# Performance work log

Measured on AMD Instinct MI355X. Metric: run time of the kernel, lower is better.

Reference implementation:

```python
import jax, jax.numpy as jnp
import numpy as np

# init kwargs baked as constants: crop_height -> depth dim, crop_length -> H, crop_width -> W
CROP_D, CROP_H, CROP_W = 16, 16, 16
EXTRAP = 0.0


def setup_inputs() -> dict:
    key = jax.random.key(0)
    k1, k2, k3 = jax.random.split(key, 3)
    N, C, D, H, W = 8, 32, 64, 64, 64
    NB = 256
    image = jax.random.normal(k1, (N, C, D, H, W), dtype=jnp.float32)
    # boxes: normalized (x1, y1, z1, x2, y2, z2) with lo <= hi per axis
    raw = jax.random.uniform(k2, (NB, 3, 2), dtype=jnp.float32)
    lo = jnp.min(raw, axis=2)
    hi = jnp.max(raw, axis=2)
    boxes = jnp.concatenate([lo, hi], axis=1)  # [NB, 6]
    box_ind = jax.random.randint(k3, (NB,), 0, N, dtype=jnp.int32)
    return {"image": image, "boxes": boxes, "box_ind": box_ind}


def _coords(lo, hi, L, c):
    # lo, hi: [nb] normalized box edges; returns [nb, c] continuous source coords
    if c > 1:
        i = jnp.arange(c, dtype=lo.dtype)
        step = (hi - lo) * (L - 1) / (c - 1)          # [nb]
        return lo[:, None] * (L - 1) + i[None, :] * step[:, None]
    return (0.5 * (lo + hi) * (L - 1))[:, None]


def _lerp_idx(coord, L):
    valid = (coord >= 0) & (coord <= L - 1)
    c = jnp.clip(coord, 0, L - 1)
    i0 = jnp.floor(c).astype(jnp.int32)
    i1 = jnp.minimum(i0 + 1, L - 1)
    frac = c - i0.astype(coord.dtype)
    return i0, i1, frac, valid


def reference(image, boxes, box_ind):
    N, C, D, H, W = image.shape
    x1, y1, z1, x2, y2, z2 = [boxes[:, k] for k in range(6)]
    zc = _coords(z1, z2, D, CROP_D)  # [nb, cd]
    yc = _coords(y1, y2, H, CROP_H)  # [nb, ch]
    xc = _coords(x1, x2, W, CROP_W)  # [nb, cw]
    z0, z1i, fz, vz = _lerp_idx(zc, D)
    y0, y1i, fy, vy = _lerp_idx(yc, H)
    x0, x1i, fx, vx = _lerp_idx(xc, W)

    img = jnp.moveaxis(image, 1, -1)  # [N, D, H, W, C] -> channels-last gather
    b = box_ind[:, None, None, None]

    def g(zi, yi, xi):
        # [nb, cd, ch, cw, C]
        return img[b, zi[:, :, None, None], yi[:, None, :, None], xi[:, None, None, :], :]

    fz_ = fz[:, :, None, None, None]
    fy_ = fy[:, None, :, None, None]
    fx_ = fx[:, None, None, :, None]

    c00 = g(z0, y0, x0) * (1 - fx_) + g(z0, y0, x1i) * fx_
    c01 = g(z0, y1i, x0) * (1 - fx_) + g(z0, y1i, x1i) * fx_
    c10 = g(z1i, y0, x0) * (1 - fx_) + g(z1i, y0, x1i) * fx_
    c11 = g(z1i, y1i, x0) * (1 - fx_) + g(z1i, y1i, x1i) * fx_
    c0 = c00 * (1 - fy_) + c01 * fy_
    c1 = c10 * (1 - fy_) + c11 * fy_
    out = c0 * (1 - fz_) + c1 * fz_  # [nb, cd, ch, cw, C]

    valid = (vz[:, :, None, None] & vy[:, None, :, None] & vx[:, None, None, :])[..., None]
    out = jnp.where(valid, out, jnp.asarray(EXTRAP, out.dtype))
    return jnp.moveaxis(out, -1, 1)  # [nb, C, cd, ch, cw]
```

## Files before the change

kernel.cpp:

```cpp
#include <hip/hip_runtime.h>
#include <stdint.h>

#define NBOX 256
#define NC   32
#define ND   64
#define NH   64
#define NW   64
#define CD   16
#define CH   16
#define CW   16
#define NXCD 8
#define DHW  (ND * NH * NW)

__global__ __launch_bounds__(NBOX) void CropAndResize3D_perm_kernel(
    const int* __restrict__ box_ind, int* __restrict__ perm)
{
    __shared__ int nsh[NBOX];
    const int t = threadIdx.x;
    nsh[t] = box_ind[t];
    __syncthreads();
    const int n_t = nsh[t];
    int rank = 0;
    #pragma unroll 8
    for (int j = 0; j < NBOX; ++j) {
        const int n_j = nsh[j];
        rank += (n_j < n_t) || (n_j == n_t && j < t);
    }
    perm[rank] = t;
}

__global__ __launch_bounds__(256) void CropAndResize3D_89481348645400_kernel(
    const float* __restrict__ image,
    const float* __restrict__ boxes,
    const int*   __restrict__ box_ind,
    const int*   __restrict__ perm,
    float*       __restrict__ out)
{
    __shared__ float sh[2 * 64 * 64];

    const int nwg_per_xcd = (NBOX * CD) / NXCD;
    const int hw  = blockIdx.x;
    const int blk = (hw & (NXCD - 1)) * nwg_per_xcd + (hw >> 3);

    const int slot = blk >> 4;
    const int b = perm ? perm[slot] : slot;
    const int z = blk & 15;
    const int t  = threadIdx.x;
    const int ty = t >> 4;
    const int tx = t & 15;

    const float bx1 = boxes[b*6+0], by1 = boxes[b*6+1], bz1 = boxes[b*6+2];
    const float bx2 = boxes[b*6+3], by2 = boxes[b*6+4], bz2 = boxes[b*6+5];
    const int   n   = box_ind[b];

    const float zstep = (bz2 - bz1) * 63.0f / 15.0f;
    const float ystep = (by2 - by1) * 63.0f / 15.0f;
    const float xstep = (bx2 - bx1) * 63.0f / 15.0f;

    const float zc = bz1 * 63.0f + (float)z * zstep;
    const bool  vz = (zc >= 0.0f) && (zc <= 63.0f);
    const float zq = fminf(fmaxf(zc, 0.0f), 63.0f);
    const int   z0 = (int)floorf(zq);
    const int   z1 = min(z0 + 1, ND - 1);
    const float fz = zq - (float)z0;

    const float yc = by1 * 63.0f + (float)ty * ystep;
    const bool  vy = (yc >= 0.0f) && (yc <= 63.0f);
    const float yq = fminf(fmaxf(yc, 0.0f), 63.0f);
    const float fy = yq - floorf(yq);

    const float xcf = bx1 * 63.0f + (float)tx * xstep;
    const bool  vx  = (xcf >= 0.0f) && (xcf <= 63.0f);
    const float xq  = fminf(fmaxf(xcf, 0.0f), 63.0f);
    const int   x0  = (int)floorf(xq);
    const int   x1  = min(x0 + 1, NW - 1);
    const float fx  = xq - (float)x0;

    const bool valid = vz && vy && vx;
    const float gz = 1.0f - fz, gy = 1.0f - fy, gx = 1.0f - fx;

    const float xcl = bx1 * 63.0f;
    const float xch = bx1 * 63.0f + 15.0f * xstep;
    const int x0min = (int)floorf(fminf(fmaxf(xcl, 0.0f), 63.0f));
    const int x1max = min((int)floorf(fminf(fmaxf(xch, 0.0f), 63.0f)) + 1, NW - 1);
    const int xlo4  = x0min & ~3;
    const int G     = ((x1max - xlo4) >> 2) + 1;

    const int key = ty & 7;
    const bool act = ((tx ^ key) < G);
    const int sx  = xlo4 + ((tx ^ key) << 2);

    int soff0, soff1, soff2, soff3;
    {
        int tmp[4];
        #pragma unroll
        for (int k = 0; k < 4; ++k) {
            const int r   = k * 16 + ty;
            const int yo  = (r >> 1) & 15;
            const int yc_ = r & 1;
            const int zs  = (r >> 5) ? z1 : z0;
            const float yco = by1 * 63.0f + (float)yo * ystep;
            const float yqs = fminf(fmaxf(yco, 0.0f), 63.0f);
            const int   ys0 = (int)floorf(yqs);
            const int   ysel = yc_ ? min(ys0 + 1, NH - 1) : ys0;
            tmp[k] = (zs * NH + ysel) * NW + sx;
        }
        soff0 = tmp[0]; soff1 = tmp[1]; soff2 = tmp[2]; soff3 = tmp[3];
    }
    const int wb    = (ty & ~3) * 64;
    const int ldsb0 = wb;
    const int ldsb1 = wb + 16 * 64;
    const int ldsb2 = wb + 32 * 64;
    const int ldsb3 = wb + 48 * 64;

    const int dx0 = x0 - xlo4;
    const int dx1 = x1 - xlo4;
    #define IDX(r, dx) ((r) * 64 + (((((dx) >> 2) ^ ((r) & 7))) << 2) + ((dx) & 3))
    const int a000 = IDX(2*ty    , dx0), a001 = IDX(2*ty    , dx1);
    const int a010 = IDX(2*ty + 1, dx0), a011 = IDX(2*ty + 1, dx1);
    const int a100 = IDX(32+2*ty , dx0), a101 = IDX(32+2*ty , dx1);
    const int a110 = IDX(33+2*ty , dx0), a111 = IDX(33+2*ty , dx1);
    #undef IDX

    const float* imgb = image + (size_t)n * (NC * DHW);
    float* op = out + (size_t)b * (NC * CD * CH * CW) + (z * CH + ty) * CW + tx;

    #define ISSUE(c)  do { if (act) {                                          \
        const float* p_ = imgb + (size_t)(c) * DHW;                            \
        float* l_ = sh + (((c) & 1) << 12);                                    \
        __builtin_amdgcn_global_load_lds(                                      \
            (const __attribute__((address_space(1))) uint32_t*)(p_ + soff0),   \
            (__attribute__((address_space(3))) uint32_t*)(l_ + ldsb0), 16, 0, 0); \
        __builtin_amdgcn_global_load_lds(                                      \
            (const __attribute__((address_space(1))) uint32_t*)(p_ + soff1),   \
            (__attribute__((address_space(3))) uint32_t*)(l_ + ldsb1), 16, 0, 0); \
        __builtin_amdgcn_global_load_lds(                                      \
            (const __attribute__((address_space(1))) uint32_t*)(p_ + soff2),   \
            (__attribute__((address_space(3))) uint32_t*)(l_ + ldsb2), 16, 0, 0); \
        __builtin_amdgcn_global_load_lds(                                      \
            (const __attribute__((address_space(1))) uint32_t*)(p_ + soff3),   \
            (__attribute__((address_space(3))) uint32_t*)(l_ + ldsb3), 16, 0, 0); \
    } } while (0)

    #define COMPUTE(c)  do {                                                   \
        const float* S_ = sh + (((c) & 1) << 12);                              \
        const float s000 = S_[a000], s001 = S_[a001];                          \
        const float s010 = S_[a010], s011 = S_[a011];                          \
        const float s100 = S_[a100], s101 = S_[a101];                          \
        const float s110 = S_[a110], s111 = S_[a111];                          \
        const float c00 = s000 * gx + s001 * fx;                               \
        const float c01 = s010 * gx + s011 * fx;                               \
        const float c10 = s100 * gx + s101 * fx;                               \
        const float c11 = s110 * gx + s111 * fx;                               \
        const float c0  = c00 * gy + c01 * fy;                                 \
        const float c1  = c10 * gy + c11 * fy;                                 \
        float v = c0 * gz + c1 * fz;                                           \
        v = valid ? v : 0.0f;                                                  \
        __builtin_nontemporal_store(v, op + (c) * (CD * CH * CW));             \
    } while (0)

    ISSUE(0);
    ISSUE(1);
    asm volatile("s_waitcnt vmcnt(4)" ::: "memory");
    __builtin_amdgcn_s_barrier();
    __builtin_amdgcn_sched_barrier(0);

    #pragma unroll 2
    for (int c = 0; c < NC; ++c) {
        COMPUTE(c);
        if (c + 1 < NC) {
            __builtin_amdgcn_sched_barrier(0);
            __builtin_amdgcn_s_barrier();
            __builtin_amdgcn_sched_barrier(0);
            if (c + 2 < NC) {
                ISSUE(c + 2);
                asm volatile("s_waitcnt vmcnt(4)" ::: "memory");
            } else {
                asm volatile("s_waitcnt vmcnt(0)" ::: "memory");
            }
            __builtin_amdgcn_sched_barrier(0);
            __builtin_amdgcn_s_barrier();
            __builtin_amdgcn_sched_barrier(0);
        }
    }

    #undef ISSUE
    #undef COMPUTE
}

extern "C" void kernel_launch(void* const* d_in, const int* in_sizes, int n_in,
                              void* d_out, int out_size, void* d_ws, size_t ws_size,
                              hipStream_t stream) {
    const float* image   = (const float*)d_in[0];
    const float* boxes   = (const float*)d_in[1];
    const int*   box_ind = (const int*)d_in[2];
    float*       out     = (float*)d_out;

    int* perm = nullptr;
    if (ws_size >= NBOX * sizeof(int)) {
        perm = (int*)d_ws;
        CropAndResize3D_perm_kernel<<<1, NBOX, 0, stream>>>(box_ind, perm);
    }

    const int blocks = NBOX * CD;
    CropAndResize3D_89481348645400_kernel<<<blocks, 256, 0, stream>>>(
        image, boxes, box_ind, perm, out);
}
```

Baseline: 112.1 us.

## Make LDS staging wave-private to drop workgroup barriers in channel loop

Remaps threads so each wave loads exactly the LDS rows it later reads (its 4 output rows across both z planes), making the double-buffered staging wave-local. This lets the per-channel s_barrier pairs be replaced with per-wave vmcnt/lgkmcnt waits, fully unrolls the loop, and has inactive lanes issue redundant clamped loads instead of being predicated off. The aim is to remove workgroup-wide synchronisation stalls, at the cost of some extra redundant global loads and a correctness dependence on exact vmcnt accounting, including the nontemporal stores.

```diff
diff --git a/kernel.cpp b/kernel.cpp
--- a/kernel.cpp
+++ b/kernel.cpp
@@ -39,15 +39,18 @@
     __shared__ float sh[2 * 64 * 64];
 
     const int nwg_per_xcd = (NBOX * CD) / NXCD;
-    const int hw  = blockIdx.x;
-    const int blk = (hw & (NXCD - 1)) * nwg_per_xcd + (hw >> 3);
+    const int hwid = blockIdx.x;
+    const int blk = (hwid & (NXCD - 1)) * nwg_per_xcd + (hwid >> 3);
 
     const int slot = blk >> 4;
     const int b = perm ? perm[slot] : slot;
     const int z = blk & 15;
     const int t  = threadIdx.x;
-    const int ty = t >> 4;
-    const int tx = t & 15;
+    const int w  = t >> 6;
+    const int l  = t & 63;
+    const int q  = l >> 4;
+    const int tx = l & 15;
+    const int ty = (w << 2) | q;
 
     const float bx1 = boxes[b*6+0], by1 = boxes[b*6+1], bz1 = boxes[b*6+2];
     const float bx2 = boxes[b*6+3], by2 = boxes[b*6+4], bz2 = boxes[b*6+5];
@@ -86,68 +89,65 @@
     const int xlo4  = x0min & ~3;
     const int G     = ((x1max - xlo4) >> 2) + 1;
 
-    const int key = ty & 7;
-    const bool act = ((tx ^ key) < G);
-    const int sx  = xlo4 + ((tx ^ key) << 2);
-
     int soff0, soff1, soff2, soff3;
     {
         int tmp[4];
         #pragma unroll
         for (int k = 0; k < 4; ++k) {
-            const int r   = k * 16 + ty;
-            const int yo  = (r >> 1) & 15;
-            const int yc_ = r & 1;
-            const int zs  = (r >> 5) ? z1 : z0;
+            const int rho = k * 4 + q;
+            const int zc_ = rho >> 3;
+            const int qq  = (rho >> 1) & 3;
+            const int yc_ = rho & 1;
+            const int zs  = zc_ ? z1 : z0;
+            const int yo  = (w << 2) | qq;
             const float yco = by1 * 63.0f + (float)yo * ystep;
             const float yqs = fminf(fmaxf(yco, 0.0f), 63.0f);
             const int   ys0 = (int)floorf(yqs);
             const int   ysel = yc_ ? min(ys0 + 1, NH - 1) : ys0;
+            const int   key = rho & 7;
+            const int   g   = tx ^ key;
+            const int   sx  = (g < G) ? (xlo4 + (g << 2)) : xlo4;
             tmp[k] = (zs * NH + ysel) * NW + sx;
         }
         soff0 = tmp[0]; soff1 = tmp[1]; soff2 = tmp[2]; soff3 = tmp[3];
     }
-    const int wb    = (ty & ~3) * 64;
-    const int ldsb0 = wb;
-    const int ldsb1 = wb + 16 * 64;
-    const int ldsb2 = wb + 32 * 64;
-    const int ldsb3 = wb + 48 * 64;
+    const int wbF = w << 10;
 
     const int dx0 = x0 - xlo4;
     const int dx1 = x1 - xlo4;
-    #define IDX(r, dx) ((r) * 64 + (((((dx) >> 2) ^ ((r) & 7))) << 2) + ((dx) & 3))
-    const int a000 = IDX(2*ty    , dx0), a001 = IDX(2*ty    , dx1);
-    const int a010 = IDX(2*ty + 1, dx0), a011 = IDX(2*ty + 1, dx1);
-    const int a100 = IDX(32+2*ty , dx0), a101 = IDX(32+2*ty , dx1);
-    const int a110 = IDX(33+2*ty , dx0), a111 = IDX(33+2*ty , dx1);
-    #undef IDX
+    #define SWZ(rho, dx) ((((((dx) >> 2) ^ ((rho) & 7))) << 2) | ((dx) & 3))
+    const int a000 = wbF + (2*q    ) * 64 + SWZ(2*q    , dx0);
+    const int a001 = wbF + (2*q    ) * 64 + SWZ(2*q    , dx1);
+    const int a010 = wbF + (2*q + 1) * 64 + SWZ(2*q + 1, dx0);
+    const int a011 = wbF + (2*q + 1) * 64 + SWZ(2*q + 1, dx1);
+    #undef SWZ
 
     const float* imgb = image + (size_t)n * (NC * DHW);
     float* op = out + (size_t)b * (NC * CD * CH * CW) + (z * CH + ty) * CW + tx;
 
-    #define ISSUE(c)  do { if (act) {                                          \
+    #define ISSUE(c)  do {                                                     \
         const float* p_ = imgb + (size_t)(c) * DHW;                            \
-        float* l_ = sh + (((c) & 1) << 12);                                    \
+        float* l_ = sh + (((c) & 1) << 12) + wbF;                              \
         __builtin_amdgcn_global_load_lds(                                      \
             (const __attribute__((address_space(1))) uint32_t*)(p_ + soff0),   \
-            (__attribute__((address_space(3))) uint32_t*)(l_ + ldsb0), 16, 0, 0); \
+            (__attribute__((address_space(3))) uint32_t*)(l_      ), 16, 0, 0);\
         __builtin_amdgcn_global_load_lds(                                      \
             (const __attribute__((address_space(1))) uint32_t*)(p_ + soff1),   \
-            (__attribute__((address_space(3))) uint32_t*)(l_ + ldsb1), 16, 0, 0); \
+            (__attribute__((address_space(3))) uint32_t*)(l_ + 256), 16, 0, 0);\
         __builtin_amdgcn_global_load_lds(                                      \
             (const __attribute__((address_space(1))) uint32_t*)(p_ + soff2),   \
-            (__attribute__((address_space(3))) uint32_t*)(l_ + ldsb2), 16, 0, 0); \
+            (__attribute__((address_space(3))) uint32_t*)(l_ + 512), 16, 0, 0);\
         __builtin_amdgcn_global_load_lds(                                      \
             (const __attribute__((address_space(1))) uint32_t*)(p_ + soff3),   \
-            (__attribute__((address_space(3))) uint32_t*)(l_ + ldsb3), 16, 0, 0); \
-    } } while (0)
+            (__attribute__((address_space(3))) uint32_t*)(l_ + 768), 16, 0, 0);\
+    } while (0)
 
     #define COMPUTE(c)  do {                                                   \
         const float* S_ = sh + (((c) & 1) << 12);                              \
-        const float s000 = S_[a000], s001 = S_[a001];                          \
-        const float s010 = S_[a010], s011 = S_[a011];                          \
-        const float s100 = S_[a100], s101 = S_[a101];                          \
-        const float s110 = S_[a110], s111 = S_[a111];                          \
+        const float s000 = S_[a000], s100 = S_[a000 + 512];                    \
+        const float s001 = S_[a001], s101 = S_[a001 + 512];                    \
+        const float s010 = S_[a010], s110 = S_[a010 + 512];                    \
+        const float s011 = S_[a011], s111 = S_[a011 + 512];                    \
         const float c00 = s000 * gx + s001 * fx;                               \
         const float c01 = s010 * gx + s011 * fx;                               \
         const float c10 = s100 * gx + s101 * fx;                               \
@@ -161,27 +161,17 @@
 
     ISSUE(0);
     ISSUE(1);
-    asm volatile("s_waitcnt vmcnt(4)" ::: "memory");
-    __builtin_amdgcn_s_barrier();
-    __builtin_amdgcn_sched_barrier(0);
 
-    #pragma unroll 2
+    #pragma unroll
     for (int c = 0; c < NC; ++c) {
+        if (c == 0)      asm volatile("s_waitcnt vmcnt(4)" ::: "memory");
+        else if (c < 31) asm volatile("s_waitcnt vmcnt(5)" ::: "memory");
+        else             asm volatile("s_waitcnt vmcnt(1)" ::: "memory");
+        __builtin_amdgcn_sched_barrier(0);
         COMPUTE(c);
-        if (c + 1 < NC) {
-            __builtin_amdgcn_sched_barrier(0);
-            __builtin_amdgcn_s_barrier();
-            __builtin_amdgcn_sched_barrier(0);
-            if (c + 2 < NC) {
-                ISSUE(c + 2);
-                asm volatile("s_waitcnt vmcnt(4)" ::: "memory");
-            } else {
-                asm volatile("s_waitcnt vmcnt(0)" ::: "memory");
-            }
-            __builtin_amdgcn_sched_barrier(0);
-            __builtin_amdgcn_s_barrier();
-            __builtin_amdgcn_sched_barrier(0);
-        }
+        asm volatile("s_waitcnt lgkmcnt(0)" ::: "memory");
+        __builtin_amdgcn_sched_barrier(0);
+        if (c + 2 < NC) ISSUE(c + 2);
     }
 
     #undef ISSUE
```

Result: slower. 120.2 us (+7.3%).
